# Performance work log

Measured on AMD Instinct MI355X. Metric: run time of the kernel, lower is better.

The kernel has to match this reference:

```python
import jax, jax.numpy as jnp
import numpy as np

N_USERS = 100000
N_ITEMS = 50000
N_NODES = N_USERS + N_ITEMS
N_EDGES = 1500000
EMBED = 100
BATCH = 4096


def spmm(rows, cols, vals, X):
    # sparse(N,N) @ dense(N,F) via gather + segment-sum
    return jax.ops.segment_sum(vals[:, None] * X[cols], rows, num_segments=N_NODES)


def setup_inputs() -> dict:
    key = jax.random.key(0)
    ks = jax.random.split(key, 24)
    userIdx = jax.random.randint(ks[0], (BATCH,), 0, N_USERS)
    itemIdx = jax.random.randint(ks[1], (BATCH,), N_USERS, N_NODES)  # offset item ids
    rows = jax.random.randint(ks[2], (N_EDGES,), 0, N_NODES)
    cols = jax.random.randint(ks[3], (N_EDGES,), 0, N_NODES)
    vals = jax.random.uniform(ks[4], (N_EDGES,), dtype=jnp.float32) * 0.01  # D^-1/2 A D^-1/2 scale
    s = 0.1
    uEmbd = jax.random.normal(ks[5], (N_USERS, EMBED), jnp.float32) * s
    iEmbd = jax.random.normal(ks[6], (N_ITEMS, EMBED), jnp.float32) * s
    # GNN layer 1: 100 -> 80 ; layer 2: 80 -> 50 (torch Linear => W stored (in,out) here)
    w1 = jax.random.normal(ks[7], (100, 80), jnp.float32) * s
    b1 = jnp.zeros((80,), jnp.float32)
    wi1 = jax.random.normal(ks[8], (100, 80), jnp.float32) * s
    bi1 = jnp.zeros((80,), jnp.float32)
    w2 = jax.random.normal(ks[9], (80, 50), jnp.float32) * s
    b2 = jnp.zeros((50,), jnp.float32)
    wi2 = jax.random.normal(ks[10], (80, 50), jnp.float32) * s
    bi2 = jnp.zeros((50,), jnp.float32)
    t1w = jax.random.normal(ks[11], (460, 64), jnp.float32) * s
    t1b = jnp.zeros((64,), jnp.float32)
    t2w = jax.random.normal(ks[12], (64, 32), jnp.float32) * s
    t2b = jnp.zeros((32,), jnp.float32)
    t3w = jax.random.normal(ks[13], (32, 1), jnp.float32) * s
    t3b = jnp.zeros((1,), jnp.float32)
    return {"userIdx": userIdx, "itemIdx": itemIdx, "rows": rows, "cols": cols,
            "vals": vals, "uEmbd": uEmbd, "iEmbd": iEmbd,
            "w1": w1, "b1": b1, "wi1": wi1, "bi1": bi1,
            "w2": w2, "b2": b2, "wi2": wi2, "bi2": bi2,
            "t1w": t1w, "t1b": t1b, "t2w": t2w, "t2b": t2b, "t3w": t3w, "t3b": t3b}


def gnn_layer(rows, cols, vals, feats, w, b, wi, bi):
    Lx = spmm(rows, cols, vals, feats)          # L @ X
    inter = Lx * feats                          # elementwise
    part1 = (Lx + feats) @ w + b                # (L + I) @ X then linear
    part2 = spmm(rows, cols, vals, inter) @ wi + bi
    return part1 + part2


def reference(userIdx, itemIdx, rows, cols, vals, uEmbd, iEmbd,
              w1, b1, wi1, bi1, w2, b2, wi2, bi2,
              t1w, t1b, t2w, t2b, t3w, t3b):
    features = jnp.concatenate([uEmbd, iEmbd], axis=0)   # [N, 100]
    final = features
    f1 = jax.nn.relu(gnn_layer(rows, cols, vals, features, w1, b1, wi1, bi1))  # [N,80]
    final = jnp.concatenate([final, f1], axis=1)
    f2 = jax.nn.relu(gnn_layer(rows, cols, vals, f1, w2, b2, wi2, bi2))        # [N,50]
    final = jnp.concatenate([final, f2], axis=1)          # [N, 230]
    embd = jnp.concatenate([final[userIdx], final[itemIdx]], axis=1)  # [B, 460]
    embd = jax.nn.relu(embd @ t1w + t1b)
    embd = embd @ t2w + t2b
    embd = embd @ t3w + t3b
    return embd.flatten()
```

## Files before the change

### kernel.cpp

```cpp
#include <hip/hip_runtime.h>

typedef unsigned int uint;
typedef unsigned short ushort_t;
typedef __attribute__((ext_vector_type(4))) float f32x4;
typedef __attribute__((ext_vector_type(8))) short bf16x8;

#define N_USERS 100000
#define N_ITEMS 50000
#define N_NODES 150000
#define N_EDGES 1500000
#define BATCH 4096
#define NSWEEP 4
#define SWEEP_ROWS 37500
#define EP_PAD 96
#define NSB 586
#define NHIST (NSB * 64)

__device__ __forceinline__ uint pack_bf16x2(float a, float b) {
    uint ua = __float_as_uint(a);
    uint ub = __float_as_uint(b);
    ua = (ua + 0x7FFFu + ((ua >> 16) & 1u)) >> 16;
    ub = (ub + 0x7FFFu + ((ub >> 16) & 1u)) >> 16;
    return ua | (ub << 16);
}
__device__ __forceinline__ ushort_t cvt_bf16(float a) {
    uint ua = __float_as_uint(a);
    return (ushort_t)((ua + 0x7FFFu + ((ua >> 16) & 1u)) >> 16);
}
__device__ __forceinline__ float bf_lo(uint u) { return __uint_as_float(u << 16); }
__device__ __forceinline__ float bf_hi(uint u) { return __uint_as_float(u & 0xFFFF0000u); }

template<int PU4>
__device__ __forceinline__ void group_gather(
    const int2* __restrict__ ep, int st, int d, int dmax,
    const uint* __restrict__ src, int l,
    float aLo[4], float aHi[4])
{
    const uint4* s4 = (const uint4*)src;
    bool lok = l < PU4;
    int2 e0 = ep[st];
    int2 e1 = ep[st + 1];
    uint4 g0 = {0u, 0u, 0u, 0u};
    if (lok && 0 < d) g0 = s4[(size_t)(uint)e0.x * PU4 + l];
    for (int j = 0; j < dmax; j++) {
        int2 e2 = ep[st + j + 2];
        uint4 g1 = {0u, 0u, 0u, 0u};
        if (lok && j + 1 < d) g1 = s4[(size_t)(uint)e1.x * PU4 + l];
        float v = (j < d) ? __int_as_float(e0.y) : 0.f;
        aLo[0] = fmaf(v, bf_lo(g0.x), aLo[0]); aHi[0] = fmaf(v, bf_hi(g0.x), aHi[0]);
        aLo[1] = fmaf(v, bf_lo(g0.y), aLo[1]); aHi[1] = fmaf(v, bf_hi(g0.y), aHi[1]);
        aLo[2] = fmaf(v, bf_lo(g0.z), aLo[2]); aHi[2] = fmaf(v, bf_hi(g0.z), aHi[2]);
        aLo[3] = fmaf(v, bf_lo(g0.w), aLo[3]); aHi[3] = fmaf(v, bf_hi(g0.w), aHi[3]);
        e0 = e1; e1 = e2; g0 = g1;
    }
}

__device__ __forceinline__ float2 row_gather_accum_mul(
    const int2* __restrict__ ep, int st, int d,
    const uint* __restrict__ sA, const uint* __restrict__ sB, int lane)
{
    constexpr int P = 40;
    float ax = 0.f, ay = 0.f;
    bool lok = lane < P;
    int2 e0 = ep[st],     e1 = ep[st + 1], e2 = ep[st + 2], e3 = ep[st + 3];
    int2 e4 = ep[st + 4], e5 = ep[st + 5];
    uint a0 = (lok && 0 < d) ? sA[(size_t)e0.x * P + lane] : 0u;
    uint c0 = (lok && 0 < d) ? sB[(size_t)e0.x * P + lane] : 0u;
    uint a1 = (lok && 1 < d) ? sA[(size_t)e1.x * P + lane] : 0u;
    uint c1 = (lok && 1 < d) ? sB[(size_t)e1.x * P + lane] : 0u;
    uint a2 = (lok && 2 < d) ? sA[(size_t)e2.x * P + lane] : 0u;
    uint c2 = (lok && 2 < d) ? sB[(size_t)e2.x * P + lane] : 0u;
    uint a3 = (lok && 3 < d) ? sA[(size_t)e3.x * P + lane] : 0u;
    uint c3 = (lok && 3 < d) ? sB[(size_t)e3.x * P + lane] : 0u;
    for (int j = 0; j < d; j += 2) {
        uint nA4 = (lok && j + 4 < d) ? sA[(size_t)e4.x * P + lane] : 0u;
        uint nC4 = (lok && j + 4 < d) ? sB[(size_t)e4.x * P + lane] : 0u;
        uint nA5 = (lok && j + 5 < d) ? sA[(size_t)e5.x * P + lane] : 0u;
        uint nC5 = (lok && j + 5 < d) ? sB[(size_t)e5.x * P + lane] : 0u;
        int2 n6 = ep[st + j + 6];
        int2 n7 = ep[st + j + 7];
        float v0 = __int_as_float(e0.y);
        ax = fmaf(v0, bf_lo(a0) * bf_lo(c0), ax);
        ay = fmaf(v0, bf_hi(a0) * bf_hi(c0), ay);
        if (j + 1 < d) {
            float v1 = __int_as_float(e1.y);
            ax = fmaf(v1, bf_lo(a1) * bf_lo(c1), ax);
            ay = fmaf(v1, bf_hi(a1) * bf_hi(c1), ay);
        }
        e0 = e2; a0 = a2; c0 = c2; e1 = e3; a1 = a3; c1 = c3;
        e2 = e4; a2 = nA4; c2 = nC4; e3 = e5; a3 = nA5; c3 = nC5;
        e4 = n6; e5 = n7;
    }
    return make_float2(ax, ay);
}

__global__ __launch_bounds__(256) void cast_feats(
    const float* __restrict__ uE, const float* __restrict__ iE,
    uint* __restrict__ Xb64, uint* __restrict__ Xc52)
{
    int g = blockIdx.x * 256 + threadIdx.x;
    if (g >= N_NODES * 64) return;
    int row = g >> 6, c = g & 63;
    uint outv = 0u;
    if (c < 50) {
        int e0 = c * 2;
        float a, b;
        if (row < N_USERS) { a = uE[(size_t)row * 100 + e0]; b = uE[(size_t)row * 100 + e0 + 1]; }
        else { a = iE[(size_t)(row - N_USERS) * 100 + e0]; b = iE[(size_t)(row - N_USERS) * 100 + e0 + 1]; }
        outv = pack_bf16x2(a, b);
    }
    Xb64[g] = outv;
    if (c < 52) Xc52[(size_t)row * 52 + c] = outv;
}

__global__ __launch_bounds__(256) void prep_weights(
    const float* __restrict__ W, const float* __restrict__ Wi,
    uint* __restrict__ wtW, uint* __restrict__ wtWi)
{
    int t = blockIdx.x * 256 + threadIdx.x;
    if (t >= 2 * 80 * 64) return;
    const float* src = (t < 80 * 64) ? W : Wi;
    uint* dst = (t < 80 * 64) ? wtW : wtWi;
    int i = t % (80 * 64);
    int col = i >> 6, kk = i & 63;
    int k = kk * 2;
    uint v = 0u;
    if (k < 100) v = pack_bf16x2(src[(size_t)k * 80 + col], src[(size_t)(k + 1) * 80 + col]);
    dst[(size_t)col * 64 + kk] = v;
}

__global__ __launch_bounds__(256) void hist_kernel(
    const int* __restrict__ rows, int* __restrict__ deg, int E)
{
    int e = blockIdx.x * 256 + threadIdx.x;
    if (e < E) atomicAdd(&deg[rows[e]], 1);
}

__global__ __launch_bounds__(256) void scan_block(
    const int* __restrict__ deg, int* __restrict__ ptr,
    int* __restrict__ bsum, int n)
{
    __shared__ int s[256];
    int t = threadIdx.x;
    int i = blockIdx.x * 256 + t;
    int v = (i < n) ? deg[i] : 0;
    s[t] = v; __syncthreads();
    for (int off = 1; off < 256; off <<= 1) {
        int x = (t >= off) ? s[t - off] : 0;
        __syncthreads();
        s[t] += x;
        __syncthreads();
    }
    if (i < n) ptr[i] = s[t] - v;
    if (t == 255) bsum[blockIdx.x] = s[255];
}

__global__ __launch_bounds__(1024) void scan_tops(int* __restrict__ bsum, int nb)
{
    __shared__ int s[1024];
    int t = threadIdx.x;
    int v = (t < nb) ? bsum[t] : 0;
    s[t] = v; __syncthreads();
    for (int off = 1; off < 1024; off <<= 1) {
        int x = (t >= off) ? s[t - off] : 0;
        __syncthreads();
        s[t] += x;
        __syncthreads();
    }
    if (t < nb) bsum[t] = s[t] - v;
}

__global__ __launch_bounds__(256) void scan_apply(
    int* __restrict__ ptr, const int* __restrict__ bsum,
    int* __restrict__ pos, int n)
{
    int i = blockIdx.x * 256 + threadIdx.x;
    if (i < n) {
        int p = ptr[i] + bsum[i >> 8];
        ptr[i] = p;
        pos[i] = p;
    }
}

__global__ __launch_bounds__(256) void scan_apply_tot(
    int* __restrict__ scanT, const int* __restrict__ bsum,
    const int* __restrict__ orig, int* __restrict__ total, int n)
{
    int i = blockIdx.x * 256 + threadIdx.x;
    if (i < n) {
        int p = scanT[i] + bsum[i >> 8];
        scanT[i] = p;
        if (total && i == n - 1) *total = p + orig[i];
    }
}

__global__ __launch_bounds__(256) void scatter_sweep(
    const int* __restrict__ rows, const int* __restrict__ cols,
    const float* __restrict__ vals, int* __restrict__ pos,
    int2* __restrict__ ep, int E, int lo, int hi)
{
    int e = blockIdx.x * 256 + threadIdx.x;
    if (e >= E) return;
    int r = rows[e];
    if (r < lo || r >= hi) return;
    int p = atomicAdd(&pos[r], 1);
    ep[p] = make_int2(cols[e], __float_as_int(vals[e]));
}

__global__ __launch_bounds__(128) void pad_ep(int2* __restrict__ ep)
{
    int t = threadIdx.x;
    if (t < EP_PAD) ep[N_EDGES + t] = make_int2(0, 0);
}

__global__ __launch_bounds__(256) void build_selmap(
    const int* __restrict__ userIdx, const int* __restrict__ itemIdx,
    int* __restrict__ selMap)
{
    int i = blockIdx.x * 256 + threadIdx.x;
    if (i < BATCH) selMap[userIdx[i]] = i;
    else if (i < 2 * BATCH) selMap[itemIdx[i - BATCH]] = i;
}

__global__ __launch_bounds__(256) void mark_needed(
    const int* __restrict__ userIdx, const int* __restrict__ itemIdx,
    const int* __restrict__ ptr_, const int* __restrict__ deg_,
    const int2* __restrict__ ep, int* __restrict__ flag)
{
    int i = blockIdx.x * 4 + ((int)threadIdx.x >> 6);
    if (i >= 2 * BATCH) return;
    int lane = threadIdx.x & 63;
    int row = (i < BATCH) ? userIdx[i] : itemIdx[i - BATCH];
    if (lane == 0) flag[row] = 1;
    int st = ptr_[row], d = deg_[row];
    for (int j = lane; j < d; j += 64)
        flag[ep[st + j].x] = 1;
}

__global__ __launch_bounds__(256) void deg_hist_blk(
    const int* __restrict__ deg, const int* __restrict__ flag,
    int* __restrict__ blockHistT, int n)
{
    __shared__ int h[64];
    int t = threadIdx.x;
    if (t < 64) h[t] = 0;
    __syncthreads();
    int i = blockIdx.x * 256 + t;
    if (i < n && (!flag || flag[i])) {
        int b = deg[i]; if (b > 63) b = 63;
        atomicAdd(&h[b], 1);
    }
    __syncthreads();
    if (t < 64) blockHistT[t * NSB + blockIdx.x] = h[t];
}

__global__ __launch_bounds__(256) void deg_scatter_blk(
    const int* __restrict__ deg, const int* __restrict__ flag,
    const int* __restrict__ scanT, int* __restrict__ sorted, int n)
{
    __shared__ int cnt[64];
    __shared__ int base[64];
    int t = threadIdx.x;
    if (t < 64) { cnt[t] = 0; base[t] = scanT[t * NSB + blockIdx.x]; }
    __syncthreads();
    int i = blockIdx.x * 256 + t;
    if (i < n && (!flag || flag[i])) {
        int b = deg[i]; if (b > 63) b = 63;
        int loc = atomicAdd(&cnt[b], 1);
        sorted[base[b] + loc] = i;
    }
}


__global__ __launch_bounds__(256) void spmm_pass1(
    const int* __restrict__ sortedAll,
    const int* __restrict__ ptr_, const int* __restrict__ deg_,
    const int2* __restrict__ ep, const uint* __restrict__ Xc,
    uint* __restrict__ B1b, uint* __restrict__ INTb, int N)
{
    int wave = (int)threadIdx.x >> 6, lane = (int)threadIdx.x & 63;
    int grp = lane >> 4, l = lane & 15;
    int si = blockIdx.x * 16 + wave * 4 + grp;
    bool valid = si < N;
    int row = valid ? sortedAll[si] : 0;
    int d = valid ? deg_[row] : 0;
    int st = valid ? ptr_[row] : 0;
    int dm = d, t;
    t = __shfl_xor(dm, 16); dm = dm > t ? dm : t;
    t = __shfl_xor(dm, 32); dm = dm > t ? dm : t;
    float aLo[4] = {0.f, 0.f, 0.f, 0.f}, aHi[4] = {0.f, 0.f, 0.f, 0.f};
    group_gather<13>(ep, st, d, dm, Xc, l, aLo, aHi);
    if (!valid) return;
    uint4 o = {0u, 0u, 0u, 0u};
    if (l < 13) {
        o.x = pack_bf16x2(aLo[0], aHi[0]); o.y = pack_bf16x2(aLo[1], aHi[1]);
        o.z = pack_bf16x2(aLo[2], aHi[2]); o.w = pack_bf16x2(aLo[3], aHi[3]);
    }
    ((uint4*)(B1b + (size_t)row * 64))[l] = o;
    if (l < 13) {
        uint4 x = ((const uint4*)(Xc + (size_t)row * 52))[l];
        uint4 p;
        p.x = pack_bf16x2(aLo[0] * bf_lo(x.x), aHi[0] * bf_hi(x.x));
        p.y = pack_bf16x2(aLo[1] * bf_lo(x.y), aHi[1] * bf_hi(x.y));
        p.z = pack_bf16x2(aLo[2] * bf_lo(x.z), aHi[2] * bf_hi(x.z));
        p.w = pack_bf16x2(aLo[3] * bf_lo(x.w), aHi[3] * bf_hi(x.w));
        ((uint4*)(INTb + (size_t)row * 52))[l] = p;
    }
}

__global__ __launch_bounds__(256) void spmm_pass2(
    const int* __restrict__ sortedAll,
    const int* __restrict__ ptr_, const int* __restrict__ deg_,
    const int2* __restrict__ ep, const uint* __restrict__ INTb,
    uint* __restrict__ B2b, int N)
{
    int wave = (int)threadIdx.x >> 6, lane = (int)threadIdx.x & 63;
    int grp = lane >> 4, l = lane & 15;
    int si = blockIdx.x * 16 + wave * 4 + grp;
    bool valid = si < N;
    int row = valid ? sortedAll[si] : 0;
    int d = valid ? deg_[row] : 0;
    int st = valid ? ptr_[row] : 0;
    int dm = d, t;
    t = __shfl_xor(dm, 16); dm = dm > t ? dm : t;
    t = __shfl_xor(dm, 32); dm = dm > t ? dm : t;
    float aLo[4] = {0.f, 0.f, 0.f, 0.f}, aHi[4] = {0.f, 0.f, 0.f, 0.f};
    group_gather<13>(ep, st, d, dm, INTb, l, aLo, aHi);
    if (!valid) return;
    uint4 o = {0u, 0u, 0u, 0u};
    if (l < 13) {
        o.x = pack_bf16x2(aLo[0], aHi[0]); o.y = pack_bf16x2(aLo[1], aHi[1]);
        o.z = pack_bf16x2(aLo[2], aHi[2]); o.w = pack_bf16x2(aLo[3], aHi[3]);
    }
    ((uint4*)(B2b + (size_t)row * 64))[l] = o;
}

__global__ __launch_bounds__(256) void spmm_pass3(
    const int* __restrict__ sorted3, const int* __restrict__ cnt3,
    const int* __restrict__ ptr_, const int* __restrict__ deg_,
    const int2* __restrict__ ep, const uint* __restrict__ F1b,
    const int* __restrict__ selMap,
    uint* __restrict__ Lxb, float* __restrict__ Lxsel)
{
    int wave = (int)threadIdx.x >> 6, lane = (int)threadIdx.x & 63;
    int grp = lane >> 4, l = lane & 15;
    int si = blockIdx.x * 16 + wave * 4 + grp;
    int n3 = *cnt3;
    bool valid = si < n3;
    int row = valid ? sorted3[si] : 0;
    int d = valid ? deg_[row] : 0;
    int st = valid ? ptr_[row] : 0;
    int dm = d, t;
    t = __shfl_xor(dm, 16); dm = dm > t ? dm : t;
    t = __shfl_xor(dm, 32); dm = dm > t ? dm : t;
    float aLo[4] = {0.f, 0.f, 0.f, 0.f}, aHi[4] = {0.f, 0.f, 0.f, 0.f};
    group_gather<10>(ep, st, d, dm, F1b, l, aLo, aHi);
    if (!valid || l >= 10) return;
    uint4 o;
    o.x = pack_bf16x2(aLo[0], aHi[0]); o.y = pack_bf16x2(aLo[1], aHi[1]);
    o.z = pack_bf16x2(aLo[2], aHi[2]); o.w = pack_bf16x2(aLo[3], aHi[3]);
    ((uint4*)(Lxb + (size_t)row * 40))[l] = o;
    int sm = selMap[row];
    if (sm >= 0) {
        float4 f0 = make_float4(aLo[0], aHi[0], aLo[1], aHi[1]);
        float4 f1 = make_float4(aLo[2], aHi[2], aLo[3], aHi[3]);
        ((float4*)(Lxsel + (size_t)sm * 80))[2 * l]     = f0;
        ((float4*)(Lxsel + (size_t)sm * 80))[2 * l + 1] = f1;
    }
}

__global__ __launch_bounds__(256) void spmm_pass4(
    const int* __restrict__ ptr_, const int* __restrict__ deg_,
    const int2* __restrict__ ep,
    const uint* __restrict__ Lxb, const uint* __restrict__ F1b,
    const int* __restrict__ userIdx, const int* __restrict__ itemIdx,
    float* __restrict__ outC)
{
    int i = blockIdx.x * 4 + ((int)threadIdx.x >> 6);
    if (i >= 2 * BATCH) return;
    int row = (i < BATCH) ? userIdx[i] : itemIdx[i - BATCH];
    int lane = threadIdx.x & 63;
    float2 r = row_gather_accum_mul(ep, ptr_[row], deg_[row], Lxb, F1b, lane);
    if (lane < 40)
        ((float2*)(outC + (size_t)i * 80))[lane] = r;
}

__global__ __launch_bounds__(256) void gemm1_mfma(
    const uint* __restrict__ B1b, const uint* __restrict__ Xb,
    const uint* __restrict__ B2b,
    const uint* __restrict__ wtW, const uint* __restrict__ wtWi,
    const float* __restrict__ b, const float* __restrict__ bi,
    const int* __restrict__ selMap,
    ushort_t* __restrict__ F1b, float* __restrict__ F1sel, int N)
{
    int wave = (int)threadIdx.x >> 6;
    int lane = (int)threadIdx.x & 63;
    int rowBase = blockIdx.x * 64 + wave * 16;
    int colLocal = lane & 15;
    int q = lane >> 4;
    int arow = rowBase + colLocal;
    bool rowOK = arow < N;

    f32x4 acc[5];
#pragma unroll
    for (int nt = 0; nt < 5; nt++) acc[nt] = (f32x4){0.f, 0.f, 0.f, 0.f};

    const bf16x8 zfrag = {};
    size_t aoff = (size_t)arow * 64 + q * 4;

#pragma unroll
    for (int ks = 0; ks < 4; ks++) {
        bf16x8 aL = rowOK ? *(const bf16x8*)(B1b + aoff + ks * 16) : zfrag;
        bf16x8 aX = rowOK ? *(const bf16x8*)(Xb  + aoff + ks * 16) : zfrag;
        bf16x8 aS = rowOK ? *(const bf16x8*)(B2b + aoff + ks * 16) : zfrag;
#pragma unroll
        for (int nt = 0; nt < 5; nt++) {
            size_t boff = (size_t)(nt * 16 + colLocal) * 64 + ks * 16 + q * 4;
            bf16x8 bW  = *(const bf16x8*)(wtW  + boff);
            bf16x8 bWi = *(const bf16x8*)(wtWi + boff);
            acc[nt] = __builtin_amdgcn_mfma_f32_16x16x32_bf16(aL, bW,  acc[nt], 0, 0, 0);
            acc[nt] = __builtin_amdgcn_mfma_f32_16x16x32_bf16(aX, bW,  acc[nt], 0, 0, 0);
            acc[nt] = __builtin_amdgcn_mfma_f32_16x16x32_bf16(aS, bWi, acc[nt], 0, 0, 0);
        }
    }

    int sm[4];
    bool rok[4];
#pragma unroll
    for (int reg = 0; reg < 4; reg++) {
        int row = rowBase + q * 4 + reg;
        rok[reg] = row < N;
        sm[reg] = rok[reg] ? selMap[row] : -1;
    }
#pragma unroll
    for (int nt = 0; nt < 5; nt++) {
        int col = nt * 16 + colLocal;
        float bias = b[col] + bi[col];
#pragma unroll
        for (int reg = 0; reg < 4; reg++) {
            if (!rok[reg]) continue;
            int row = rowBase + q * 4 + reg;
            float v = fmaxf(acc[nt][reg] + bias, 0.f);
            F1b[(size_t)row * 80 + col] = cvt_bf16(v);
            if (sm[reg] >= 0) F1sel[(size_t)sm[reg] * 80 + col] = v;
        }
    }
}

__global__ __launch_bounds__(256) void gemm_fused2_sel(
    const float* __restrict__ Lxsel, const float* __restrict__ F1sel,
    const int* __restrict__ selMap,
    const float* __restrict__ S2c,
    const float* __restrict__ W, const float* __restrict__ b,
    const float* __restrict__ Wi, const float* __restrict__ bi,
    const int* __restrict__ userIdx, const int* __restrict__ itemIdx,
    float* __restrict__ outC)
{
    constexpr int K = 80, M = 50, TPR = 2, MT = M / TPR;
    __shared__ float sW[K * M];
    __shared__ float sWi[K * M];
    for (int i = threadIdx.x; i < K * M; i += 256) {
        sW[i]  = W[i];
        sWi[i] = Wi[i];
    }
    __syncthreads();

    int i = blockIdx.x * (256 / TPR) + (int)threadIdx.x / TPR;
    int mBase = ((int)threadIdx.x % TPR) * MT;
    if (i >= 2 * BATCH) return;
    int r = (i < BATCH) ? userIdx[i] : itemIdx[i - BATCH];
    int sm = selMap[r];

    const float* xrow = F1sel + (size_t)sm * K;
    const float* lrow = Lxsel + (size_t)sm * K;
    const float* srow = S2c + (size_t)i * K;

    float acc[MT];
#pragma unroll
    for (int m = 0; m < MT; m++) acc[m] = 0.0f;

    for (int k4 = 0; k4 < K; k4 += 4) {
        float4 lv = *(const float4*)(lrow + k4);
        float4 xv = *(const float4*)(xrow + k4);
        float4 sv = *(const float4*)(srow + k4);
        float a[4] = {lv.x + xv.x, lv.y + xv.y, lv.z + xv.z, lv.w + xv.w};
        float s[4] = {sv.x, sv.y, sv.z, sv.w};
#pragma unroll
        for (int kk = 0; kk < 4; kk++) {
            const float* wk  = &sW[(k4 + kk) * M + mBase];
            const float* wik = &sWi[(k4 + kk) * M + mBase];
#pragma unroll
            for (int m = 0; m < MT; m++)
                acc[m] = fmaf(a[kk], wk[m], fmaf(s[kk], wik[m], acc[m]));
        }
    }

    float* orow = outC + (size_t)i * M + mBase;
#pragma unroll
    for (int m = 0; m < MT; m++)
        orow[m] = fmaxf(acc[m] + b[mBase + m] + bi[mBase + m], 0.0f);
}

template<int K, int M, int TPR, bool RELU>
__global__ __launch_bounds__(256) void mlp_gemm(
    const float* __restrict__ A,
    const float* __restrict__ W, const float* __restrict__ b,
    float* __restrict__ out, int N)
{
    __shared__ float sW[K * M];
    for (int i = threadIdx.x; i < K * M; i += 256) sW[i] = W[i];
    __syncthreads();

    constexpr int RPB = 256 / TPR;
    constexpr int MT  = M / TPR;
    int r = blockIdx.x * RPB + (int)threadIdx.x / TPR;
    int mBase = ((int)threadIdx.x % TPR) * MT;
    if (r >= N) return;

    const float* arow = A + (size_t)r * K;
    float acc[MT];
#pragma unroll
    for (int m = 0; m < MT; m++) acc[m] = 0.0f;

    for (int k = 0; k < K; k++) {
        float a = arow[k];
#pragma unroll
        for (int m = 0; m < MT; m++)
            acc[m] = fmaf(a, sW[k * M + mBase + m], acc[m]);
    }

    float* orow = out + (size_t)r * M + mBase;
#pragma unroll
    for (int m = 0; m < MT; m++) {
        float vv = acc[m] + b[mBase + m];
        orow[m] = RELU ? fmaxf(vv, 0.0f) : vv;
    }
}

__global__ __launch_bounds__(128) void gather_embd(
    const int* __restrict__ userIdx, const int* __restrict__ itemIdx,
    const float* __restrict__ uE, const float* __restrict__ iE,
    const float* __restrict__ F1sel, const int* __restrict__ selMap,
    const float* __restrict__ f2c,
    float* __restrict__ emb)
{
    int bi = blockIdx.x;
    int u  = userIdx[bi];
    int it = itemIdx[bi];
    int su = selMap[u];
    int si = selMap[it];
    float* orow = emb + (size_t)bi * 460;
    for (int c = threadIdx.x; c < 460; c += 128) {
        float val;
        if (c < 100) {
            val = (u < N_USERS) ? uE[(size_t)u * 100 + c]
                                : iE[(size_t)(u - N_USERS) * 100 + c];
        } else if (c < 180) {
            val = F1sel[(size_t)su * 80 + (c - 100)];
        } else if (c < 230) {
            val = f2c[(size_t)bi * 50 + (c - 180)];
        } else if (c < 330) {
            int cc = c - 230;
            val = (it < N_USERS) ? uE[(size_t)it * 100 + cc]
                                 : iE[(size_t)(it - N_USERS) * 100 + cc];
        } else if (c < 410) {
            val = F1sel[(size_t)si * 80 + (c - 330)];
        } else {
            val = f2c[(size_t)(BATCH + bi) * 50 + (c - 410)];
        }
        orow[c] = val;
    }
}

extern "C" void kernel_launch(void* const* d_in, const int* in_sizes, int n_in,
                              void* d_out, int out_size, void* d_ws, size_t ws_size,
                              hipStream_t stream) {
    const int*   userIdx = (const int*)d_in[0];
    const int*   itemIdx = (const int*)d_in[1];
    const int*   rows    = (const int*)d_in[2];
    const int*   cols    = (const int*)d_in[3];
    const float* vals    = (const float*)d_in[4];
    const float* uEmbd   = (const float*)d_in[5];
    const float* iEmbd   = (const float*)d_in[6];
    const float* w1      = (const float*)d_in[7];
    const float* b1      = (const float*)d_in[8];
    const float* wi1     = (const float*)d_in[9];
    const float* bi1     = (const float*)d_in[10];
    const float* w2      = (const float*)d_in[11];
    const float* b2      = (const float*)d_in[12];
    const float* wi2     = (const float*)d_in[13];
    const float* bi2     = (const float*)d_in[14];
    const float* t1w     = (const float*)d_in[15];
    const float* t1b     = (const float*)d_in[16];
    const float* t2w     = (const float*)d_in[17];
    const float* t2b     = (const float*)d_in[18];
    const float* t3w     = (const float*)d_in[19];
    const float* t3b     = (const float*)d_in[20];

    float* ws = (float*)d_ws;
    uint*  Xb64  = (uint*)ws;
    uint*  Xc52  = (uint*)(ws + 9600000);
    uint*  B1b   = (uint*)(ws + 17400000);
    uint*  Lxb   = B1b;
    uint*  INTb  = (uint*)(ws + 27000000);
    uint*  F1b   = INTb;
    uint*  B2b   = (uint*)(ws + 34800000);
    uint*  wtW   = (uint*)(ws + 44400000);
    uint*  wtWi  = (uint*)(ws + 44405120);
    float* F1sel = ws + 44410240;
    float* Lxsel = ws + 45065600;
    float* B2c   = ws + 45720960;
    float* F2c   = ws + 46376320;
    float* EMB   = ws + 46785920;
    float* H1    = ws + 48670080;
    float* H2    = ws + 48932224;
    int*   deg   = (int*)(ws + 49063296);
    int*   ptr   = deg + 150000;
    int*   pos   = ptr + 150000;
    int*   bsum  = pos + 150000;
    int2*  ep    = (int2*)(bsum + 1024);
    int*   flag  = (int*)(ep + 1500096);
    int*   selMap= flag + 150000;
    int*   sortedAll = selMap + 150000;
    int*   sorted3   = sortedAll + 150000;
    int*   blockHistT= sorted3 + 150000;
    int*   scanT     = blockHistT + NHIST;
    int*   bsum3     = scanT + NHIST;
    int*   cnt3      = bsum3 + 1024;

    const int E = N_EDGES;
    dim3 blk(256);

    cast_feats<<<(N_NODES * 64 + 255) / 256, blk, 0, stream>>>(uEmbd, iEmbd, Xb64, Xc52);
    prep_weights<<<(2 * 80 * 64 + 255) / 256, blk, 0, stream>>>(w1, wi1, wtW, wtWi);

    hipMemsetAsync(deg, 0, 150000 * sizeof(int), stream);
    hipMemsetAsync(flag, 0, 150000 * sizeof(int), stream);
    hipMemsetAsync(selMap, 0xFF, 150000 * sizeof(int), stream);
    hist_kernel<<<(E + 255) / 256, blk, 0, stream>>>(rows, deg, E);
    int nScanBlocks = NSB;
    scan_block<<<nScanBlocks, blk, 0, stream>>>(deg, ptr, bsum, N_NODES);
    scan_tops<<<1, dim3(1024), 0, stream>>>(bsum, nScanBlocks);
    scan_apply<<<nScanBlocks, blk, 0, stream>>>(ptr, bsum, pos, N_NODES);
    for (int s = 0; s < NSWEEP; s++) {
        scatter_sweep<<<(E + 255) / 256, blk, 0, stream>>>(
            rows, cols, vals, pos, ep, E, s * SWEEP_ROWS, (s + 1) * SWEEP_ROWS);
    }
    pad_ep<<<1, dim3(128), 0, stream>>>(ep);

    build_selmap<<<(2 * BATCH + 255) / 256, blk, 0, stream>>>(userIdx, itemIdx, selMap);
    mark_needed<<<(2 * BATCH + 3) / 4, blk, 0, stream>>>(
        userIdx, itemIdx, ptr, deg, ep, flag);

    int nHistBlocks = (NHIST + 255) / 256;
    deg_hist_blk<<<nScanBlocks, blk, 0, stream>>>(deg, nullptr, blockHistT, N_NODES);
    scan_block<<<nHistBlocks, blk, 0, stream>>>(blockHistT, scanT, bsum3, NHIST);
    scan_tops<<<1, dim3(1024), 0, stream>>>(bsum3, nHistBlocks);
    scan_apply_tot<<<nHistBlocks, blk, 0, stream>>>(scanT, bsum3, blockHistT, nullptr, NHIST);
    deg_scatter_blk<<<nScanBlocks, blk, 0, stream>>>(deg, nullptr, scanT, sortedAll, N_NODES);
    deg_hist_blk<<<nScanBlocks, blk, 0, stream>>>(deg, flag, blockHistT, N_NODES);
    scan_block<<<nHistBlocks, blk, 0, stream>>>(blockHistT, scanT, bsum3, NHIST);
    scan_tops<<<1, dim3(1024), 0, stream>>>(bsum3, nHistBlocks);
    scan_apply_tot<<<nHistBlocks, blk, 0, stream>>>(scanT, bsum3, blockHistT, cnt3, NHIST);
    deg_scatter_blk<<<nScanBlocks, blk, 0, stream>>>(deg, flag, scanT, sorted3, N_NODES);

    int grpGrid = (N_NODES + 15) / 16;
    int selGrid = (2 * BATCH + 3) / 4;

    spmm_pass1<<<grpGrid, blk, 0, stream>>>(
        sortedAll, ptr, deg, ep, Xc52, B1b, INTb, N_NODES);
    spmm_pass2<<<grpGrid, blk, 0, stream>>>(
        sortedAll, ptr, deg, ep, INTb, B2b, N_NODES);
    {
        int grid = (N_NODES + 63) / 64;
        gemm1_mfma<<<grid, blk, 0, stream>>>(
            B1b, Xb64, B2b, wtW, wtWi, b1, bi1, selMap,
            (ushort_t*)F1b, F1sel, N_NODES);
    }

    spmm_pass3<<<grpGrid, blk, 0, stream>>>(
        sorted3, cnt3, ptr, deg, ep, F1b, selMap, Lxb, Lxsel);
    spmm_pass4<<<selGrid, blk, 0, stream>>>(
        ptr, deg, ep, Lxb, F1b, userIdx, itemIdx, B2c);
    {
        int grid = (2 * BATCH + 127) / 128;
        gemm_fused2_sel<<<grid, blk, 0, stream>>>(
            Lxsel, F1sel, selMap, B2c, w2, b2, wi2, bi2, userIdx, itemIdx, F2c);
    }

    gather_embd<<<BATCH, dim3(128), 0, stream>>>(
        userIdx, itemIdx, uEmbd, iEmbd, F1sel, selMap, F2c, EMB);
    {
        constexpr int TPR = 8;
        int grid = (BATCH + (256 / TPR) - 1) / (256 / TPR);
        mlp_gemm<460, 64, TPR, true><<<grid, blk, 0, stream>>>(
            EMB, t1w, t1b, H1, BATCH);
    }
    {
        constexpr int TPR = 4;
        int grid = (BATCH + (256 / TPR) - 1) / (256 / TPR);
        mlp_gemm<64, 32, TPR, false><<<grid, blk, 0, stream>>>(
            H1, t2w, t2b, H2, BATCH);
    }
    {
        constexpr int TPR = 1;
        int grid = (BATCH + 255) / 256;
        mlp_gemm<32, 1, TPR, false><<<grid, blk, 0, stream>>>(
            H2, t3w, t3b, (float*)d_out, BATCH);
    }
}
```

Before: 556.0 us.

## Store layer-1 SpMM gather sources in scaled FP8 with 8-lane row groups

Features and the intermediate product used by the first two SpMM passes are stored as FP8 (e4m3) with power-of-two scaling instead of bf16, halving the bytes gathered per neighbour. Each row is now handled by 8 lanes holding 16 features apiece, so 32 rows fit per block, and the wave-wide max-degree loop is replaced by a per-lane loop over the row's own degree. A separate cast kernel produces the FP8 copy. The cost is much lower precision on the gathered operands, which may push results past the accuracy tolerance, plus extra unpack/convert ALU work.

```diff
diff --git a/kernel.cpp b/kernel.cpp
--- a/kernel.cpp
+++ b/kernel.cpp
@@ -3,6 +3,7 @@
 typedef unsigned int uint;
 typedef unsigned short ushort_t;
 typedef __attribute__((ext_vector_type(4))) float f32x4;
+typedef __attribute__((ext_vector_type(2))) float f32x2;
 typedef __attribute__((ext_vector_type(8))) short bf16x8;
 
 #define N_USERS 100000
@@ -29,6 +30,48 @@
 }
 __device__ __forceinline__ float bf_lo(uint u) { return __uint_as_float(u << 16); }
 __device__ __forceinline__ float bf_hi(uint u) { return __uint_as_float(u & 0xFFFF0000u); }
+
+__device__ __forceinline__ uint pack_fp8x4(float a, float b, float c, float d) {
+    uint r = 0;
+    r = (uint)__builtin_amdgcn_cvt_pk_fp8_f32(a, b, (int)r, false);
+    r = (uint)__builtin_amdgcn_cvt_pk_fp8_f32(c, d, (int)r, true);
+    return r;
+}
+__device__ __forceinline__ void unpack_fp8x4(uint u, float o[4]) {
+    f32x2 lo = __builtin_amdgcn_cvt_pk_f32_fp8((int)u, false);
+    f32x2 hi = __builtin_amdgcn_cvt_pk_f32_fp8((int)u, true);
+    o[0] = lo.x; o[1] = lo.y; o[2] = hi.x; o[3] = hi.y;
+}
+
+__device__ __forceinline__ void gather8_fp8(
+    const int2* __restrict__ ep, int st, int d,
+    const uint4* __restrict__ s4, int l, float acc[16])
+{
+    int2 e0 = ep[st];
+    int2 e1 = ep[st + 1];
+    uint4 g0 = {0u, 0u, 0u, 0u};
+    if (0 < d) g0 = s4[(size_t)(uint)e0.x * 8 + l];
+    for (int j = 0; j < d; j++) {
+        int2 e2 = ep[st + j + 2];
+        uint4 g1 = {0u, 0u, 0u, 0u};
+        if (j + 1 < d) g1 = s4[(size_t)(uint)e1.x * 8 + l];
+        float v = __int_as_float(e0.y);
+        float f[4];
+        unpack_fp8x4(g0.x, f);
+#pragma unroll
+        for (int k = 0; k < 4; k++) acc[k]      = fmaf(v, f[k], acc[k]);
+        unpack_fp8x4(g0.y, f);
+#pragma unroll
+        for (int k = 0; k < 4; k++) acc[4 + k]  = fmaf(v, f[k], acc[4 + k]);
+        unpack_fp8x4(g0.z, f);
+#pragma unroll
+        for (int k = 0; k < 4; k++) acc[8 + k]  = fmaf(v, f[k], acc[8 + k]);
+        unpack_fp8x4(g0.w, f);
+#pragma unroll
+        for (int k = 0; k < 4; k++) acc[12 + k] = fmaf(v, f[k], acc[12 + k]);
+        e0 = e1; e1 = e2; g0 = g1;
+    }
+}
 
 template<int PU4>
 __device__ __forceinline__ void group_gather(
@@ -96,7 +139,7 @@
 
 __global__ __launch_bounds__(256) void cast_feats(
     const float* __restrict__ uE, const float* __restrict__ iE,
-    uint* __restrict__ Xb64, uint* __restrict__ Xc52)
+    uint* __restrict__ Xb64)
 {
     int g = blockIdx.x * 256 + threadIdx.x;
     if (g >= N_NODES * 64) return;
@@ -110,7 +153,24 @@
         outv = pack_bf16x2(a, b);
     }
     Xb64[g] = outv;
-    if (c < 52) Xc52[(size_t)row * 52 + c] = outv;
+}
+
+__global__ __launch_bounds__(256) void cast_fp8(
+    const float* __restrict__ uE, const float* __restrict__ iE,
+    uint* __restrict__ Xf8)
+{
+    int g = blockIdx.x * 256 + threadIdx.x;
+    if (g >= N_NODES * 32) return;
+    int row = g >> 5, c = g & 31;
+    uint outv = 0u;
+    int f0 = c * 4;
+    if (f0 < 100) {
+        const float* src = (row < N_USERS) ? (uE + (size_t)row * 100)
+                                           : (iE + (size_t)(row - N_USERS) * 100);
+        outv = pack_fp8x4(src[f0] * 16.f, src[f0 + 1] * 16.f,
+                          src[f0 + 2] * 16.f, src[f0 + 3] * 16.f);
+    }
+    Xf8[g] = outv;
 }
 
 __global__ __launch_bounds__(256) void prep_weights(
@@ -275,64 +335,71 @@
 __global__ __launch_bounds__(256) void spmm_pass1(
     const int* __restrict__ sortedAll,
     const int* __restrict__ ptr_, const int* __restrict__ deg_,
-    const int2* __restrict__ ep, const uint* __restrict__ Xc,
-    uint* __restrict__ B1b, uint* __restrict__ INTb, int N)
+    const int2* __restrict__ ep, const uint* __restrict__ Xf8,
+    uint* __restrict__ B1b, uint* __restrict__ INTf8, int N)
 {
     int wave = (int)threadIdx.x >> 6, lane = (int)threadIdx.x & 63;
-    int grp = lane >> 4, l = lane & 15;
-    int si = blockIdx.x * 16 + wave * 4 + grp;
+    int grp = lane >> 3, l = lane & 7;
+    int si = blockIdx.x * 32 + wave * 8 + grp;
     bool valid = si < N;
     int row = valid ? sortedAll[si] : 0;
     int d = valid ? deg_[row] : 0;
     int st = valid ? ptr_[row] : 0;
-    int dm = d, t;
-    t = __shfl_xor(dm, 16); dm = dm > t ? dm : t;
-    t = __shfl_xor(dm, 32); dm = dm > t ? dm : t;
-    float aLo[4] = {0.f, 0.f, 0.f, 0.f}, aHi[4] = {0.f, 0.f, 0.f, 0.f};
-    group_gather<13>(ep, st, d, dm, Xc, l, aLo, aHi);
+    float acc[16];
+#pragma unroll
+    for (int k = 0; k < 16; k++) acc[k] = 0.f;
+    gather8_fp8(ep, st, d, (const uint4*)Xf8, l, acc);
     if (!valid) return;
-    uint4 o = {0u, 0u, 0u, 0u};
-    if (l < 13) {
-        o.x = pack_bf16x2(aLo[0], aHi[0]); o.y = pack_bf16x2(aLo[1], aHi[1]);
-        o.z = pack_bf16x2(aLo[2], aHi[2]); o.w = pack_bf16x2(aLo[3], aHi[3]);
-    }
-    ((uint4*)(B1b + (size_t)row * 64))[l] = o;
-    if (l < 13) {
-        uint4 x = ((const uint4*)(Xc + (size_t)row * 52))[l];
-        uint4 p;
-        p.x = pack_bf16x2(aLo[0] * bf_lo(x.x), aHi[0] * bf_hi(x.x));
-        p.y = pack_bf16x2(aLo[1] * bf_lo(x.y), aHi[1] * bf_hi(x.y));
-        p.z = pack_bf16x2(aLo[2] * bf_lo(x.z), aHi[2] * bf_hi(x.z));
-        p.w = pack_bf16x2(aLo[3] * bf_lo(x.w), aHi[3] * bf_hi(x.w));
-        ((uint4*)(INTb + (size_t)row * 52))[l] = p;
-    }
+
+    uint u[8];
+#pragma unroll
+    for (int k = 0; k < 8; k++)
+        u[k] = pack_bf16x2(acc[2 * k] * 0.0625f, acc[2 * k + 1] * 0.0625f);
+    uint4* bdst = (uint4*)(B1b + (size_t)row * 64 + l * 8);
+    bdst[0] = make_uint4(u[0], u[1], u[2], u[3]);
+    bdst[1] = make_uint4(u[4], u[5], u[6], u[7]);
+
+    uint4 xs4 = ((const uint4*)(Xf8 + (size_t)row * 32))[l];
+    float xs[16];
+    unpack_fp8x4(xs4.x, xs); unpack_fp8x4(xs4.y, xs + 4);
+    unpack_fp8x4(xs4.z, xs + 8); unpack_fp8x4(xs4.w, xs + 12);
+    float t[16];
+#pragma unroll
+    for (int k = 0; k < 16; k++) t[k] = 16.f * acc[k] * xs[k];
+    uint4 o;
+    o.x = pack_fp8x4(t[0], t[1], t[2], t[3]);
+    o.y = pack_fp8x4(t[4], t[5], t[6], t[7]);
+    o.z = pack_fp8x4(t[8], t[9], t[10], t[11]);
+    o.w = pack_fp8x4(t[12], t[13], t[14], t[15]);
+    ((uint4*)(INTf8 + (size_t)row * 32))[l] = o;
 }
 
 __global__ __launch_bounds__(256) void spmm_pass2(
     const int* __restrict__ sortedAll,
     const int* __restrict__ ptr_, const int* __restrict__ deg_,
-    const int2* __restrict__ ep, const uint* __restrict__ INTb,
+    const int2* __restrict__ ep, const uint* __restrict__ INTf8,
     uint* __restrict__ B2b, int N)
 {
     int wave = (int)threadIdx.x >> 6, lane = (int)threadIdx.x & 63;
-    int grp = lane >> 4, l = lane & 15;
-    int si = blockIdx.x * 16 + wave * 4 + grp;
+    int grp = lane >> 3, l = lane & 7;
+    int si = blockIdx.x * 32 + wave * 8 + grp;
     bool valid = si < N;
     int row = valid ? sortedAll[si] : 0;
     int d = valid ? deg_[row] : 0;
     int st = valid ? ptr_[row] : 0;
-    int dm = d, t;
-    t = __shfl_xor(dm, 16); dm = dm > t ? dm : t;
-    t = __shfl_xor(dm, 32); dm = dm > t ? dm : t;
-    float aLo[4] = {0.f, 0.f, 0.f, 0.f}, aHi[4] = {0.f, 0.f, 0.f, 0.f};
-    group_gather<13>(ep, st, d, dm, INTb, l, aLo, aHi);
+    float acc[16];
+#pragma unroll
+    for (int k = 0; k < 16; k++) acc[k] = 0.f;
+    gather8_fp8(ep, st, d, (const uint4*)INTf8, l, acc);
     if (!valid) return;
-    uint4 o = {0u, 0u, 0u, 0u};
-    if (l < 13) {
-        o.x = pack_bf16x2(aLo[0], aHi[0]); o.y = pack_bf16x2(aLo[1], aHi[1]);
-        o.z = pack_bf16x2(aLo[2], aHi[2]); o.w = pack_bf16x2(aLo[3], aHi[3]);
-    }
-    ((uint4*)(B2b + (size_t)row * 64))[l] = o;
+    const float DS = 1.f / 4096.f;
+    uint u[8];
+#pragma unroll
+    for (int k = 0; k < 8; k++)
+        u[k] = pack_bf16x2(acc[2 * k] * DS, acc[2 * k + 1] * DS);
+    uint4* bdst = (uint4*)(B2b + (size_t)row * 64 + l * 8);
+    bdst[0] = make_uint4(u[0], u[1], u[2], u[3]);
+    bdst[1] = make_uint4(u[4], u[5], u[6], u[7]);
 }
 
 __global__ __launch_bounds__(256) void spmm_pass3(
@@ -599,11 +666,11 @@
 
     float* ws = (float*)d_ws;
     uint*  Xb64  = (uint*)ws;
-    uint*  Xc52  = (uint*)(ws + 9600000);
-    uint*  B1b   = (uint*)(ws + 17400000);
+    uint*  Xf8   = (uint*)(ws + 9600000);
+    uint*  B1b   = (uint*)(ws + 14400000);
     uint*  Lxb   = B1b;
-    uint*  INTb  = (uint*)(ws + 27000000);
-    uint*  F1b   = INTb;
+    uint*  INTf8 = (uint*)(ws + 24000000);
+    uint*  F1b   = (uint*)(ws + 28800000);
     uint*  B2b   = (uint*)(ws + 34800000);
     uint*  wtW   = (uint*)(ws + 44400000);
     uint*  wtWi  = (uint*)(ws + 44405120);
@@ -631,7 +698,8 @@
     const int E = N_EDGES;
     dim3 blk(256);
 
-    cast_feats<<<(N_NODES * 64 + 255) / 256, blk, 0, stream>>>(uEmbd, iEmbd, Xb64, Xc52);
+    cast_feats<<<(N_NODES * 64 + 255) / 256, blk, 0, stream>>>(uEmbd, iEmbd, Xb64);
+    cast_fp8<<<(N_NODES * 32 + 255) / 256, blk, 0, stream>>>(uEmbd, iEmbd, Xf8);
     prep_weights<<<(2 * 80 * 64 + 255) / 256, blk, 0, stream>>>(w1, wi1, wtW, wtWi);
 
     hipMemsetAsync(deg, 0, 150000 * sizeof(int), stream);
@@ -664,13 +732,14 @@
     scan_apply_tot<<<nHistBlocks, blk, 0, stream>>>(scanT, bsum3, blockHistT, cnt3, NHIST);
     deg_scatter_blk<<<nScanBlocks, blk, 0, stream>>>(deg, flag, scanT, sorted3, N_NODES);
 
-    int grpGrid = (N_NODES + 15) / 16;
-    int selGrid = (2 * BATCH + 3) / 4;
-
-    spmm_pass1<<<grpGrid, blk, 0, stream>>>(
-        sortedAll, ptr, deg, ep, Xc52, B1b, INTb, N_NODES);
-    spmm_pass2<<<grpGrid, blk, 0, stream>>>(
-        sortedAll, ptr, deg, ep, INTb, B2b, N_NODES);
+    int grpGrid8 = (N_NODES + 31) / 32;
+    int grpGrid  = (N_NODES + 15) / 16;
+    int selGrid  = (2 * BATCH + 3) / 4;
+
+    spmm_pass1<<<grpGrid8, blk, 0, stream>>>(
+        sortedAll, ptr, deg, ep, Xf8, B1b, INTf8, N_NODES);
+    spmm_pass2<<<grpGrid8, blk, 0, stream>>>(
+        sortedAll, ptr, deg, ep, INTf8, B2b, N_NODES);
     {
         int grid = (N_NODES + 63) / 64;
         gemm1_mfma<<<grid, blk, 0, stream>>>(
```

Measured after the change: 504.3 us. 1.1x faster.
